# Kernel optimization log

Hardware: AMD Instinct MI355X
Metric: run time of the kernel (lower is better)

## Reference

```python
import jax, jax.numpy as jnp
import numpy as np

B, S, D, H = 4, 2048, 1024, 16
HD = D // H
EPS = 1e-5


def setup_inputs() -> dict:
    key = jax.random.key(0)
    ks = jax.random.split(key, 12)
    scale = 1.0 / np.sqrt(D)
    inp = {
        "x": jax.random.normal(ks[0], (B, S, D), dtype=jnp.float32),
        "template_ids": jax.random.randint(ks[1], (B, S), 0, 1000, dtype=jnp.int64)
            if jax.config.jax_enable_x64 else jax.random.randint(ks[1], (B, S), 0, 1000, dtype=jnp.int32),
        "attention_mask": jnp.ones((B, S), dtype=jnp.int32),
        "Wq": jax.random.normal(ks[2], (D, D), dtype=jnp.float32) * scale,
        "bq": jnp.zeros((D,), dtype=jnp.float32),
        "Wk": jax.random.normal(ks[3], (D, D), dtype=jnp.float32) * scale,
        "bk": jnp.zeros((D,), dtype=jnp.float32),
        "Wv": jax.random.normal(ks[4], (D, D), dtype=jnp.float32) * scale,
        "bv": jnp.zeros((D,), dtype=jnp.float32),
        "Wo": jax.random.normal(ks[5], (D, D), dtype=jnp.float32) * scale,
        "bo": jnp.zeros((D,), dtype=jnp.float32),
        "gamma": jnp.ones((D,), dtype=jnp.float32),
        "beta": jnp.zeros((D,), dtype=jnp.float32),
    }
    return inp


def _split_heads(t):
    # [B,S,D] -> [B,H,S,HD]
    return t.reshape(B, S, H, HD).transpose(0, 2, 1, 3)


def reference(x, template_ids, attention_mask, Wq, bq, Wk, bk, Wv, bv, Wo, bo, gamma, beta):
    q = _split_heads(x @ Wq.T + bq)
    k = _split_heads(x @ Wk.T + bk)
    v = _split_heads(x @ Wv.T + bv)
    # [B,H,S,S]
    scores = jnp.einsum("bhqd,bhkd->bhqk", q, k) / jnp.sqrt(jnp.float32(HD))
    mask = attention_mask[:, None, None, :]  # broadcast over heads and query dim
    scores = jnp.where(mask == 0, jnp.float32(-10000.0), scores)
    attn = jax.nn.softmax(scores, axis=-1)  # dropout is identity in eval
    out = jnp.einsum("bhqk,bhkd->bhqd", attn, v)
    out = out.transpose(0, 2, 1, 3).reshape(B, S, D)
    out = out @ Wo.T + bo
    # residual + LayerNorm
    y = x + out
    mu = jnp.mean(y, axis=-1, keepdims=True)
    var = jnp.var(y, axis=-1, keepdims=True)
    return (y - mu) * jax.lax.rsqrt(var + EPS) * gamma + beta
```

## Files before the change

kernel.cpp:

```cpp
#include <hip/hip_runtime.h>

typedef unsigned short u16;
typedef unsigned int u32;
typedef __attribute__((ext_vector_type(8))) short bf16x8;
typedef __attribute__((ext_vector_type(4))) float f32x4;

#define NB 4
#define SS 2048
#define DD 1024
#define NH 16
#define HD 64
#define MM (NB*SS)

struct __align__(16) Pack16 { unsigned int w0, w1, w2, w3; };
union PU { Pack16 p; u16 s[8]; };

__device__ __forceinline__ float b2f(u16 u) {
    union { unsigned int i; float f; } v; v.i = ((unsigned int)u) << 16; return v.f;
}
__device__ __forceinline__ u16 f2b(float f) {
    union { unsigned int i; float f; } v; v.f = f;
    return (u16)((v.i + 0x7FFFu + ((v.i >> 16) & 1u)) >> 16);
}
__device__ __forceinline__ u32 packbf(float a, float b) {
    u32 ia = __float_as_uint(a), ib = __float_as_uint(b);
    return ((ia + 0x8000u) >> 16) | ((ib + 0x8000u) & 0xFFFF0000u);
}
__device__ __forceinline__ float rdS(const void* p, size_t i, int mode) {
    return mode ? ((const float*)p)[i] : b2f(((const u16*)p)[i]);
}
__device__ __forceinline__ float ex2(float x) { return __builtin_amdgcn_exp2f(x); }

__device__ __forceinline__ void cp16(const u16* g, u16* l) {
    __builtin_amdgcn_global_load_lds(
        (const __attribute__((address_space(1))) void*)g,
        (__attribute__((address_space(3))) void*)l, 16, 0, 0);
}

__device__ __forceinline__ void pl32swap(u32& a, u32& b) {
    asm volatile("v_permlane32_swap_b32 %0, %1" : "+v"(a), "+v"(b));
}
__device__ __forceinline__ void pl16swap(u32& a, u32& b) {
    asm volatile("v_permlane16_swap_b32 %0, %1" : "+v"(a), "+v"(b));
}

#define QSC 0.1803368801111204f
#define GX ((size_t)MM * DD / 8)
#define GW ((size_t)DD * DD / 8)
#define GTOT (GX + 4 * GW + 512)

__global__ __launch_bounds__(256) void convert_kernel(
    const void* __restrict__ x,
    const void* __restrict__ Wq, const void* __restrict__ Wk,
    const void* __restrict__ Wv, const void* __restrict__ Wo,
    const void* __restrict__ bq, const void* __restrict__ bk,
    const void* __restrict__ bv, const void* __restrict__ bo,
    u16* __restrict__ xb, u16* __restrict__ Wc, u16* __restrict__ Wob,
    u16* __restrict__ bcat, const u32* __restrict__ gamma_w)
{
    const int mode = (gamma_w[0] == 0x3F800000u) ? 1 : 0;
    size_t g = (size_t)blockIdx.x * 256 + threadIdx.x;
    const void* src; u16* dst; size_t off; float sc = 1.0f;
    if (g < GX)               { src = x;  dst = xb;              off = g * 8; }
    else if (g < GX + GW)     { src = Wq; dst = Wc;              off = (g - GX) * 8; sc = QSC; }
    else if (g < GX + 2 * GW) { src = Wk; dst = Wc + (size_t)DD * DD;     off = (g - GX - GW) * 8; }
    else if (g < GX + 3 * GW) { src = Wv; dst = Wc + (size_t)2 * DD * DD; off = (g - GX - 2 * GW) * 8; }
    else if (g < GX + 4 * GW) { src = Wo; dst = Wob;             off = (g - GX - 3 * GW) * 8; }
    else {
        size_t gg = g - (GX + 4 * GW);
        int which = (int)(gg >> 7); off = (gg & 127) * 8;
        src = (which == 0) ? bq : (which == 1) ? bk : (which == 2) ? bv : bo;
        dst = bcat + which * DD;
        if (which == 0) sc = QSC;
    }
    PU o;
    if (mode) {
        const float* s = (const float*)src + off;
        float4 a = ((const float4*)s)[0];
        float4 b = ((const float4*)s)[1];
        o.s[0] = f2b(a.x * sc); o.s[1] = f2b(a.y * sc);
        o.s[2] = f2b(a.z * sc); o.s[3] = f2b(a.w * sc);
        o.s[4] = f2b(b.x * sc); o.s[5] = f2b(b.y * sc);
        o.s[6] = f2b(b.z * sc); o.s[7] = f2b(b.w * sc);
    } else {
        PU in; in.p = *(const Pack16*)((const u16*)src + off);
#pragma unroll
        for (int j = 0; j < 8; j++) o.s[j] = f2b(b2f(in.s[j]) * sc);
    }
    *(Pack16*)(dst + off) = o.p;
}

__global__ __launch_bounds__(256) void gemm_qkv(
    const u16* __restrict__ xb, const u16* __restrict__ Wc, const u16* __restrict__ bcat,
    u16* __restrict__ Q, u16* __restrict__ K, u16* __restrict__ V)
{
    __shared__ __align__(16) u16 sh[2 * 128 * 64];
    u16* As = sh;
    u16* Bs = sh + 128 * 64;

    const int tid  = threadIdx.x;
    const int wv   = tid >> 6;
    const int lane = tid & 63;
    const int wy = wv >> 1, wx = wv & 1;
    const int l15 = lane & 15, quad = lane >> 4;
    const int m0 = blockIdx.x * 128, n0 = blockIdx.y * 128;
    const int srow = lane >> 3;
    const int sw   = ((lane & 7) ^ srow) * 8;
    const int key  = l15 & 7;

    f32x4 acc[4][4];
#pragma unroll
    for (int i = 0; i < 4; i++)
#pragma unroll
        for (int j = 0; j < 4; j++) acc[i][j] = (f32x4){0.f, 0.f, 0.f, 0.f};

    for (int k0 = 0; k0 < DD; k0 += 64) {
#pragma unroll
        for (int c = 0; c < 4; c++) {
            cp16(&xb[(size_t)(m0 + wv * 32 + c * 8 + srow) * DD + k0 + sw],
                 &As[wv * 2048 + c * 512]);
            cp16(&Wc[(size_t)(n0 + wv * 32 + c * 8 + srow) * DD + k0 + sw],
                 &Bs[wv * 2048 + c * 512]);
        }
        __syncthreads();
#pragma unroll
        for (int ks = 0; ks < 2; ks++) {
            bf16x8 a[4], bb[4];
#pragma unroll
            for (int mt = 0; mt < 4; mt++)
                a[mt] = *(const bf16x8*)&As[(wy * 64 + mt * 16 + l15) * 64 +
                                            (((ks << 2) + quad) ^ key) * 8];
#pragma unroll
            for (int nt = 0; nt < 4; nt++)
                bb[nt] = *(const bf16x8*)&Bs[(wx * 64 + nt * 16 + l15) * 64 +
                                             (((ks << 2) + quad) ^ key) * 8];
#pragma unroll
            for (int mt = 0; mt < 4; mt++)
#pragma unroll
                for (int nt = 0; nt < 4; nt++)
                    acc[mt][nt] = __builtin_amdgcn_mfma_f32_16x16x32_bf16(
                        a[mt], bb[nt], acc[mt][nt], 0, 0, 0);
        }
        __syncthreads();
    }

    const int z = n0 >> 10;
    if (z != 2) {
        u16* out = (z == 0) ? Q : K;
#pragma unroll
        for (int nt = 0; nt < 4; nt++) {
            int n_g = n0 + wx * 64 + nt * 16 + l15;
            float bv_ = b2f(bcat[n_g]);
            int nn = n_g & 1023;
            int h = nn >> 6, hd = nn & 63;
#pragma unroll
            for (int mt = 0; mt < 4; mt++) {
#pragma unroll
                for (int r = 0; r < 4; r++) {
                    int m_g = m0 + wy * 64 + mt * 16 + quad * 4 + r;
                    int b = m_g >> 11, s = m_g & (SS - 1);
                    out[(((size_t)(b * NH + h) * SS) + s) * HD + hd] =
                        f2b(acc[mt][nt][r] + bv_);
                }
            }
        }
    } else {
        const int bb_ = m0 >> 11, sbase = m0 & (SS - 1);
#pragma unroll
        for (int ph = 0; ph < 2; ph++) {
            if (wx == ph) {
#pragma unroll
                for (int nt = 0; nt < 4; nt++) {
                    int n_loc = nt * 16 + l15;
                    float bv_ = b2f(bcat[n0 + ph * 64 + n_loc]);
#pragma unroll
                    for (int mt = 0; mt < 4; mt++) {
                        int m = wy * 64 + mt * 16 + quad * 4;
                        uint2 wr;
                        wr.x = (u32)f2b(acc[mt][nt][0] + bv_) |
                               ((u32)f2b(acc[mt][nt][1] + bv_) << 16);
                        wr.y = (u32)f2b(acc[mt][nt][2] + bv_) |
                               ((u32)f2b(acc[mt][nt][3] + bv_) << 16);
                        *(uint2*)&sh[n_loc * 136 + m] = wr;
                    }
                }
            }
            __syncthreads();
            {
                int row = tid >> 2;
                int sg  = tid & 3;
                int n_g = n0 + ph * 64 + row;
                int nn = n_g & 1023;
                int h = nn >> 6, hd = nn & 63;
                u16* dst = &V[(((size_t)(bb_ * NH + h)) * HD + hd) * SS + sbase];
#pragma unroll
                for (int j = 0; j < 4; j++) {
                    int mloc = sg * 32 + j * 8;
                    *(Pack16*)&dst[mloc] = *(const Pack16*)&sh[row * 136 + mloc];
                }
            }
            __syncthreads();
        }
    }
}

__global__ __launch_bounds__(256, 4) void attn_kernel(
    const u16* __restrict__ Q, const u16* __restrict__ K, const u16* __restrict__ V,
    const int* __restrict__ mask, u16* __restrict__ O)
{
    const int bh = blockIdx.y;
    const int b = bh >> 4, h = bh & 15;
    const int q0 = blockIdx.x * 128;
    const u16* Qp  = Q + (size_t)bh * SS * HD;
    const u16* Kp  = K + (size_t)bh * SS * HD;
    const u16* Vtg = V + (size_t)bh * HD * SS;
    const int* mk = mask + b * SS;

    __shared__ __align__(16) u16 Kl[2 * 64 * 64];
    __shared__ __align__(16) u16 Vt[2 * 64 * 64];
    __shared__ int s_anymask;

    const int tid  = threadIdx.x;
    const int w    = tid >> 6;
    const int lane = tid & 63;
    const int l15 = lane & 15, quad = lane >> 4;
    const int srow = lane >> 3;
    const int sw   = ((lane & 7) ^ srow) * 8;
    const int key  = l15 & 7;

    if (tid == 0) s_anymask = 0;
    __syncthreads();
    {
        int local = 0;
#pragma unroll
        for (int i = 0; i < 2; i++) {
            int4 m4 = ((const int4*)mk)[i * 256 + tid];
            if ((m4.x == 0) | (m4.y == 0) | (m4.z == 0) | (m4.w == 0)) local = 1;
        }
        if (local) s_anymask = 1;
    }
    __syncthreads();
    const bool anymask = (s_anymask != 0);

    bf16x8 qf[2][2];
#pragma unroll
    for (int qt = 0; qt < 2; qt++)
#pragma unroll
        for (int ks = 0; ks < 2; ks++)
            qf[qt][ks] = *(const bf16x8*)&Qp[(size_t)(q0 + w * 32 + qt * 16 + l15) * HD +
                                             ks * 32 + quad * 8];

    f32x4 oacc[2][4];
#pragma unroll
    for (int i = 0; i < 2; i++)
#pragma unroll
        for (int j = 0; j < 4; j++) oacc[i][j] = (f32x4){0.f, 0.f, 0.f, 0.f};

    float lsum[2] = {0.f, 0.f};

#pragma unroll
    for (int c = 0; c < 2; c++) {
        cp16(&Kp[(size_t)(w * 16 + c * 8 + srow) * HD + sw], &Kl[w * 1024 + c * 512]);
        cp16(&Vtg[(size_t)(w * 16 + c * 8 + srow) * SS + sw], &Vt[w * 1024 + c * 512]);
    }

    for (int it = 0; it < SS / 64; it++) {
        const int kv0 = it * 64;
        const int p = it & 1;
        __syncthreads();

        if (it + 1 < SS / 64) {
            const int kn = kv0 + 64;
#pragma unroll
            for (int c = 0; c < 2; c++) {
                cp16(&Kp[(size_t)(kn + w * 16 + c * 8 + srow) * HD + sw],
                     &Kl[(p ^ 1) * 4096 + w * 1024 + c * 512]);
                cp16(&Vtg[(size_t)(w * 16 + c * 8 + srow) * SS + kn + sw],
                     &Vt[(p ^ 1) * 4096 + w * 1024 + c * 512]);
            }
        }

        f32x4 sacc[4][2];
#pragma unroll
        for (int i = 0; i < 4; i++)
#pragma unroll
            for (int j = 0; j < 2; j++) sacc[i][j] = (f32x4){0.f, 0.f, 0.f, 0.f};
#pragma unroll
        for (int ks = 0; ks < 2; ks++) {
            bf16x8 kf[4];
#pragma unroll
            for (int kvt = 0; kvt < 4; kvt++)
                kf[kvt] = *(const bf16x8*)&Kl[p * 4096 + (kvt * 16 + l15) * 64 +
                                              (((ks << 2) + quad) ^ key) * 8];
            __builtin_amdgcn_s_setprio(1);
#pragma unroll
            for (int kvt = 0; kvt < 4; kvt++)
#pragma unroll
                for (int qt = 0; qt < 2; qt++)
                    sacc[kvt][qt] = __builtin_amdgcn_mfma_f32_16x16x32_bf16(
                        kf[kvt], qf[qt][ks], sacc[kvt][qt], 0, 0, 0);
            __builtin_amdgcn_s_setprio(0);
        }

        union { bf16x8 v; u32 d[4]; } paf[2][2];
#pragma unroll
        for (int qt = 0; qt < 2; qt++) {
            u32 pk[4][2];
#pragma unroll
            for (int kvt = 0; kvt < 4; kvt++) {
                f32x4 vv = sacc[kvt][qt];
                if (anymask) {
#pragma unroll
                    for (int r = 0; r < 4; r++) {
                        int kv = kv0 + kvt * 16 + quad * 4 + r;
                        if (mk[kv] == 0) vv[r] = -20000.0f;
                    }
                }
                float p0 = ex2(vv[0]);
                float p1 = ex2(vv[1]);
                float p2 = ex2(vv[2]);
                float p3 = ex2(vv[3]);
                lsum[qt] += (p0 + p1) + (p2 + p3);
                pk[kvt][0] = packbf(p0, p1);
                pk[kvt][1] = packbf(p2, p3);
            }
#pragma unroll
            for (int ks2 = 0; ks2 < 2; ks2++) {
#pragma unroll
                for (int c = 0; c < 2; c++) {
                    u32 x0 = pk[ks2 * 2 + 0][c];
                    u32 x1 = pk[ks2 * 2 + 1][c];
                    pl32swap(x0, x1);
                    pl16swap(x0, x1);
                    paf[qt][ks2].d[c]     = x0;
                    paf[qt][ks2].d[2 + c] = x1;
                }
            }
        }

#pragma unroll
        for (int ks2 = 0; ks2 < 2; ks2++) {
            bf16x8 vf[4];
#pragma unroll
            for (int nt = 0; nt < 4; nt++)
                vf[nt] = *(const bf16x8*)&Vt[p * 4096 + (nt * 16 + l15) * 64 +
                                             (((ks2 << 2) + quad) ^ key) * 8];
            __builtin_amdgcn_s_setprio(1);
#pragma unroll
            for (int qt = 0; qt < 2; qt++) {
#pragma unroll
                for (int nt = 0; nt < 4; nt++)
                    oacc[qt][nt] = __builtin_amdgcn_mfma_f32_16x16x32_bf16(
                        paf[qt][ks2].v, vf[nt], oacc[qt][nt], 0, 0, 0);
            }
            __builtin_amdgcn_s_setprio(0);
        }
    }

#pragma unroll
    for (int qt = 0; qt < 2; qt++) {
        lsum[qt] += __shfl_xor(lsum[qt], 16, 64);
        lsum[qt] += __shfl_xor(lsum[qt], 32, 64);
    }
#pragma unroll
    for (int qt = 0; qt < 2; qt++) {
#pragma unroll
        for (int r = 0; r < 4; r++) {
            float inv = 1.0f / __shfl(lsum[qt], quad * 4 + r, 64);
            int row = q0 + w * 32 + qt * 16 + quad * 4 + r;
            size_t base = ((size_t)(b * SS + row)) * DD + h * HD;
#pragma unroll
            for (int nt = 0; nt < 4; nt++)
                O[base + nt * 16 + l15] = f2b(oacc[qt][nt][r] * inv);
        }
    }
}

__global__ __launch_bounds__(256) void gemm_oproj(
    const u16* __restrict__ A, const u16* __restrict__ Wob, const u16* __restrict__ bcat,
    u16* __restrict__ Y)
{
    __shared__ __align__(16) u16 As[128 * 64];
    __shared__ __align__(16) u16 Bs[128 * 64];

    const int tid  = threadIdx.x;
    const int wv   = tid >> 6;
    const int lane = tid & 63;
    const int wy = wv >> 1, wx = wv & 1;
    const int l15 = lane & 15, quad = lane >> 4;
    const int m0 = blockIdx.x * 128, n0 = blockIdx.y * 128;
    const int srow = lane >> 3;
    const int sw   = ((lane & 7) ^ srow) * 8;
    const int key  = l15 & 7;

    f32x4 acc[4][4];
#pragma unroll
    for (int i = 0; i < 4; i++)
#pragma unroll
        for (int j = 0; j < 4; j++) acc[i][j] = (f32x4){0.f, 0.f, 0.f, 0.f};

    for (int k0 = 0; k0 < DD; k0 += 64) {
#pragma unroll
        for (int c = 0; c < 4; c++) {
            cp16(&A[(size_t)(m0 + wv * 32 + c * 8 + srow) * DD + k0 + sw],
                 &As[wv * 2048 + c * 512]);
            cp16(&Wob[(size_t)(n0 + wv * 32 + c * 8 + srow) * DD + k0 + sw],
                 &Bs[wv * 2048 + c * 512]);
        }
        __syncthreads();
#pragma unroll
        for (int ks = 0; ks < 2; ks++) {
            bf16x8 a[4], bb[4];
#pragma unroll
            for (int mt = 0; mt < 4; mt++)
                a[mt] = *(const bf16x8*)&As[(wy * 64 + mt * 16 + l15) * 64 +
                                            (((ks << 2) + quad) ^ key) * 8];
#pragma unroll
            for (int nt = 0; nt < 4; nt++)
                bb[nt] = *(const bf16x8*)&Bs[(wx * 64 + nt * 16 + l15) * 64 +
                                             (((ks << 2) + quad) ^ key) * 8];
#pragma unroll
            for (int mt = 0; mt < 4; mt++)
#pragma unroll
                for (int nt = 0; nt < 4; nt++)
                    acc[mt][nt] = __builtin_amdgcn_mfma_f32_16x16x32_bf16(
                        a[mt], bb[nt], acc[mt][nt], 0, 0, 0);
        }
        __syncthreads();
    }

#pragma unroll
    for (int nt = 0; nt < 4; nt++) {
        int n_g = n0 + wx * 64 + nt * 16 + l15;
        float bv_ = b2f(bcat[3 * DD + n_g]);
#pragma unroll
        for (int mt = 0; mt < 4; mt++) {
#pragma unroll
            for (int r = 0; r < 4; r++) {
                int m_g = m0 + wy * 64 + mt * 16 + quad * 4 + r;
                Y[(size_t)m_g * DD + n_g] = f2b(acc[mt][nt][r] + bv_);
            }
        }
    }
}

__global__ __launch_bounds__(256) void ln_kernel(
    const u16* __restrict__ Yp, const void* __restrict__ x,
    const void* __restrict__ gamma, const void* __restrict__ beta,
    void* __restrict__ out)
{
    const int mode = (((const u32*)gamma)[0] == 0x3F800000u) ? 1 : 0;
    const int w    = threadIdx.x >> 6;
    const int lane = threadIdx.x & 63;
    const int row  = blockIdx.x * 4 + w;
    const u16* y = Yp + (size_t)row * DD;

    float vals[16];
    float s = 0.f, sq = 0.f;
#pragma unroll
    for (int i = 0; i < 2; i++) {
        PU d; d.p = *(const Pack16*)&y[i * 512 + lane * 8];
        if (mode) {
            const float* xp = (const float*)x + (size_t)row * DD + i * 512 + lane * 8;
            float4 xa = ((const float4*)xp)[0];
            float4 xb2 = ((const float4*)xp)[1];
            float xr[8] = {xa.x, xa.y, xa.z, xa.w, xb2.x, xb2.y, xb2.z, xb2.w};
#pragma unroll
            for (int j = 0; j < 8; j++) {
                float f = b2f(d.s[j]) + xr[j];
                vals[i * 8 + j] = f;
                s += f; sq += f * f;
            }
        } else {
            const u16* xp = (const u16*)x + (size_t)row * DD + i * 512 + lane * 8;
            PU xd; xd.p = *(const Pack16*)xp;
#pragma unroll
            for (int j = 0; j < 8; j++) {
                float f = b2f(d.s[j]) + b2f(xd.s[j]);
                vals[i * 8 + j] = f;
                s += f; sq += f * f;
            }
        }
    }
#pragma unroll
    for (int off = 1; off < 64; off <<= 1) {
        s  += __shfl_xor(s, off);
        sq += __shfl_xor(sq, off);
    }
    float mu  = s * (1.0f / 1024.0f);
    float var = sq * (1.0f / 1024.0f) - mu * mu;
    float rs  = rsqrtf(var + 1e-5f);

#pragma unroll
    for (int i = 0; i < 2; i++) {
        float r8[8];
#pragma unroll
        for (int j = 0; j < 8; j++) {
            int col = i * 512 + lane * 8 + j;
            r8[j] = (vals[i * 8 + j] - mu) * rs * rdS(gamma, col, mode) + rdS(beta, col, mode);
        }
        if (mode) {
            float* of = (float*)out + (size_t)row * DD + i * 512 + lane * 8;
            ((float4*)of)[0] = make_float4(r8[0], r8[1], r8[2], r8[3]);
            ((float4*)of)[1] = make_float4(r8[4], r8[5], r8[6], r8[7]);
        } else {
            PU ob;
#pragma unroll
            for (int j = 0; j < 8; j++) ob.s[j] = f2b(r8[j]);
            *(Pack16*)((u16*)out + (size_t)row * DD + i * 512 + lane * 8) = ob.p;
        }
    }
}

extern "C" void kernel_launch(void* const* d_in, const int* in_sizes, int n_in,
                              void* d_out, int out_size, void* d_ws, size_t ws_size,
                              hipStream_t stream)
{
    const void* x     = d_in[0];
    const int* mask   = (const int*)d_in[2];
    const void* Wq    = d_in[3];
    const void* bq    = d_in[4];
    const void* Wk    = d_in[5];
    const void* bk    = d_in[6];
    const void* Wv    = d_in[7];
    const void* bv    = d_in[8];
    const void* Wo    = d_in[9];
    const void* bo    = d_in[10];
    const void* gamma = d_in[11];
    const void* beta  = d_in[12];

    const size_t n = (size_t)MM * DD;
    u16* xb   = (u16*)((char*)d_ws + 256);
    u16* Wc   = xb + n;
    u16* Wob  = Wc + (size_t)3 * DD * DD;
    u16* bcat = Wob + (size_t)DD * DD;
    u16* Qb   = bcat + 4096;
    u16* Kb   = Qb + n;
    u16* Vb   = Kb + n;
    u16* Ab   = Vb + n;
    u16* Yb   = xb;

    convert_kernel<<<(unsigned)(GTOT / 256), 256, 0, stream>>>(
        x, Wq, Wk, Wv, Wo, bq, bk, bv, bo, xb, Wc, Wob, bcat, (const u32*)gamma);
    gemm_qkv<<<dim3(MM / 128, 3 * DD / 128), 256, 0, stream>>>(xb, Wc, bcat, Qb, Kb, Vb);
    attn_kernel<<<dim3(SS / 128, NB * NH), 256, 0, stream>>>(Qb, Kb, Vb, mask, Ab);
    gemm_oproj<<<dim3(MM / 128, DD / 128), 256, 0, stream>>>(Ab, Wob, bcat, Yb);
    ln_kernel<<<MM / 4, 256, 0, stream>>>(Yb, x, gamma, beta, d_out);
}
```

Baseline: 327.5 us.

## Rewrite QKV and output GEMMs as 256x128 triple-buffered pipelined tiles

Replaces the two 128x128 single-buffered GEMM loops with a shared 256x128 tile routine run by 512 threads. It uses three LDS stages with async global-to-LDS loads two tiles ahead, split A/B staging, explicit vmcnt waits, sched barriers and setprio around the MFMA blocks. The grids are remapped with an XCD-aware block swizzle, and the V transpose epilogue is done in one pass. The aim is to hide global-load latency and raise reuse per block, at the cost of more LDS per block (144KB), lower occupancy and fragile hand-placed wait counts.

Result: slower. 351.2 us (+7.2%).

```diff
diff --git a/kernel.cpp b/kernel.cpp
--- a/kernel.cpp
+++ b/kernel.cpp
@@ -43,6 +43,8 @@
 __device__ __forceinline__ void pl16swap(u32& a, u32& b) {
     asm volatile("v_permlane16_swap_b32 %0, %1" : "+v"(a), "+v"(b));
 }
+
+#define SBAR __builtin_amdgcn_sched_barrier(0)
 
 #define QSC 0.1803368801111204f
 #define GX ((size_t)MM * DD / 8)
@@ -90,66 +92,133 @@
     *(Pack16*)(dst + off) = o.p;
 }
 
-__global__ __launch_bounds__(256) void gemm_qkv(
-    const u16* __restrict__ xb, const u16* __restrict__ Wc, const u16* __restrict__ bcat,
-    u16* __restrict__ Q, u16* __restrict__ K, u16* __restrict__ V)
-{
-    __shared__ __align__(16) u16 sh[2 * 128 * 64];
-    u16* As = sh;
-    u16* Bs = sh + 128 * 64;
-
+__device__ __forceinline__ void mfma_tile_256x128(
+    const u16* __restrict__ Ag,
+    const u16* __restrict__ Bg,
+    u16* sh, f32x4 (&acc)[4][4])
+{
     const int tid  = threadIdx.x;
     const int wv   = tid >> 6;
     const int lane = tid & 63;
-    const int wy = wv >> 1, wx = wv & 1;
+    const int wm = wv >> 1, wn = wv & 1;
     const int l15 = lane & 15, quad = lane >> 4;
-    const int m0 = blockIdx.x * 128, n0 = blockIdx.y * 128;
     const int srow = lane >> 3;
     const int sw   = ((lane & 7) ^ srow) * 8;
     const int key  = l15 & 7;
-
-    f32x4 acc[4][4];
-#pragma unroll
-    for (int i = 0; i < 4; i++)
-#pragma unroll
-        for (int j = 0; j < 4; j++) acc[i][j] = (f32x4){0.f, 0.f, 0.f, 0.f};
-
-    for (int k0 = 0; k0 < DD; k0 += 64) {
-#pragma unroll
-        for (int c = 0; c < 4; c++) {
-            cp16(&xb[(size_t)(m0 + wv * 32 + c * 8 + srow) * DD + k0 + sw],
-                 &As[wv * 2048 + c * 512]);
-            cp16(&Wc[(size_t)(n0 + wv * 32 + c * 8 + srow) * DD + k0 + sw],
-                 &Bs[wv * 2048 + c * 512]);
-        }
-        __syncthreads();
-#pragma unroll
-        for (int ks = 0; ks < 2; ks++) {
-            bf16x8 a[4], bb[4];
-#pragma unroll
-            for (int mt = 0; mt < 4; mt++)
-                a[mt] = *(const bf16x8*)&As[(wy * 64 + mt * 16 + l15) * 64 +
-                                            (((ks << 2) + quad) ^ key) * 8];
-#pragma unroll
-            for (int nt = 0; nt < 4; nt++)
-                bb[nt] = *(const bf16x8*)&Bs[(wx * 64 + nt * 16 + l15) * 64 +
-                                             (((ks << 2) + quad) ^ key) * 8];
-#pragma unroll
-            for (int mt = 0; mt < 4; mt++)
+    const int NT   = DD / 64;
+
+#define QSTAGE_A(tt, cc) do { \
+    const u16* s_ = Ag + (size_t)(tt) * 64; \
+    const int lb_ = (cc) * 24576 + wv * 1024; \
+    cp16(s_ + (size_t)(wv * 16 +           srow) * DD + sw, &sh[lb_]); \
+    cp16(s_ + (size_t)(wv * 16 + 8 +       srow) * DD + sw, &sh[lb_ + 512]); \
+    cp16(s_ + (size_t)(128 + wv * 16 +     srow) * DD + sw, &sh[lb_ + 8192]); \
+    cp16(s_ + (size_t)(128 + wv * 16 + 8 + srow) * DD + sw, &sh[lb_ + 8704]); \
+} while (0)
+#define QSTAGE_B(tt, cc) do { \
+    const u16* s_ = Bg + (size_t)(tt) * 64; \
+    const int lb_ = (cc) * 24576 + 16384 + wv * 1024; \
+    cp16(s_ + (size_t)(wv * 16 +     srow) * DD + sw, &sh[lb_]); \
+    cp16(s_ + (size_t)(wv * 16 + 8 + srow) * DD + sw, &sh[lb_ + 512]); \
+} while (0)
+
+    QSTAGE_A(0, 0); QSTAGE_B(0, 0);
+    QSTAGE_A(1, 1); QSTAGE_B(1, 1);
+    SBAR;
+    asm volatile("s_waitcnt vmcnt(6)");
+    __builtin_amdgcn_s_barrier();
+    SBAR;
+
+    int cb = 0;
+    for (int t = 0; t < NT; ++t) {
+        const int c2 = (cb >= 1) ? cb - 1 : 2;
+        const int ab = cb * 24576;
+        const int bb = ab + 16384;
+
+        bf16x8 bfr[4][2], afr[2][2];
+#pragma unroll
+        for (int nt = 0; nt < 4; nt++)
+#pragma unroll
+            for (int ks = 0; ks < 2; ks++)
+                bfr[nt][ks] = *(const bf16x8*)&sh[bb + (wn * 64 + nt * 16 + l15) * 64 +
+                                                  (((ks << 2) + quad) ^ key) * 8];
+#pragma unroll
+        for (int mt = 0; mt < 2; mt++)
+#pragma unroll
+            for (int ks = 0; ks < 2; ks++)
+                afr[mt][ks] = *(const bf16x8*)&sh[ab + (wm * 64 + mt * 16 + l15) * 64 +
+                                                  (((ks << 2) + quad) ^ key) * 8];
+        if (t + 2 < NT) QSTAGE_A(t + 2, c2);
+        SBAR; __builtin_amdgcn_s_barrier(); SBAR;
+        __builtin_amdgcn_s_setprio(1);
+#pragma unroll
+        for (int ks = 0; ks < 2; ks++)
+#pragma unroll
+            for (int mt = 0; mt < 2; mt++)
 #pragma unroll
                 for (int nt = 0; nt < 4; nt++)
                     acc[mt][nt] = __builtin_amdgcn_mfma_f32_16x16x32_bf16(
-                        a[mt], bb[nt], acc[mt][nt], 0, 0, 0);
-        }
-        __syncthreads();
-    }
+                        afr[mt][ks], bfr[nt][ks], acc[mt][nt], 0, 0, 0);
+        __builtin_amdgcn_s_setprio(0);
+        SBAR; __builtin_amdgcn_s_barrier(); SBAR;
+
+#pragma unroll
+        for (int mt = 0; mt < 2; mt++)
+#pragma unroll
+            for (int ks = 0; ks < 2; ks++)
+                afr[mt][ks] = *(const bf16x8*)&sh[ab + (wm * 64 + 32 + mt * 16 + l15) * 64 +
+                                                  (((ks << 2) + quad) ^ key) * 8];
+        if (t + 2 < NT) QSTAGE_B(t + 2, c2);
+        SBAR; __builtin_amdgcn_s_barrier(); SBAR;
+        __builtin_amdgcn_s_setprio(1);
+#pragma unroll
+        for (int ks = 0; ks < 2; ks++)
+#pragma unroll
+            for (int mt = 0; mt < 2; mt++)
+#pragma unroll
+                for (int nt = 0; nt < 4; nt++)
+                    acc[2 + mt][nt] = __builtin_amdgcn_mfma_f32_16x16x32_bf16(
+                        afr[mt][ks], bfr[nt][ks], acc[2 + mt][nt], 0, 0, 0);
+        __builtin_amdgcn_s_setprio(0);
+        SBAR;
+        if (t + 2 < NT)      asm volatile("s_waitcnt vmcnt(6)");
+        else if (t + 1 < NT) asm volatile("s_waitcnt vmcnt(0)");
+        __builtin_amdgcn_s_barrier();
+        SBAR;
+        cb = (cb == 2) ? 0 : cb + 1;
+    }
+#undef QSTAGE_A
+#undef QSTAGE_B
+}
+
+__global__ __launch_bounds__(512, 2) void gemm_qkv(
+    const u16* __restrict__ xb, const u16* __restrict__ Wc, const u16* __restrict__ bcat,
+    u16* __restrict__ Q, u16* __restrict__ K, u16* __restrict__ V)
+{
+    __shared__ __align__(16) u16 sh[3 * 24576];
+    const int wg = (blockIdx.x & 7) * 96 + (blockIdx.x >> 3);
+    const int mb = wg & 31, nb = wg >> 5;
+    const int m0 = mb * 256, n0 = nb * 128;
+
+    f32x4 acc[4][4];
+#pragma unroll
+    for (int i = 0; i < 4; i++)
+#pragma unroll
+        for (int j = 0; j < 4; j++) acc[i][j] = (f32x4){0.f, 0.f, 0.f, 0.f};
+
+    mfma_tile_256x128(xb + (size_t)m0 * DD, Wc + (size_t)n0 * DD, sh, acc);
+
+    const int tid = threadIdx.x;
+    const int wv = tid >> 6, lane = tid & 63;
+    const int wm = wv >> 1, wn = wv & 1;
+    const int l15 = lane & 15, quad = lane >> 4;
 
     const int z = n0 >> 10;
     if (z != 2) {
         u16* out = (z == 0) ? Q : K;
 #pragma unroll
         for (int nt = 0; nt < 4; nt++) {
-            int n_g = n0 + wx * 64 + nt * 16 + l15;
+            int n_g = n0 + wn * 64 + nt * 16 + l15;
             float bv_ = b2f(bcat[n_g]);
             int nn = n_g & 1023;
             int h = nn >> 6, hd = nn & 63;
@@ -157,7 +226,7 @@
             for (int mt = 0; mt < 4; mt++) {
 #pragma unroll
                 for (int r = 0; r < 4; r++) {
-                    int m_g = m0 + wy * 64 + mt * 16 + quad * 4 + r;
+                    int m_g = m0 + wm * 64 + mt * 16 + quad * 4 + r;
                     int b = m_g >> 11, s = m_g & (SS - 1);
                     out[(((size_t)(b * NH + h) * SS) + s) * HD + hd] =
                         f2b(acc[mt][nt][r] + bv_);
@@ -165,41 +234,36 @@
             }
         }
     } else {
-        const int bb_ = m0 >> 11, sbase = m0 & (SS - 1);
-#pragma unroll
-        for (int ph = 0; ph < 2; ph++) {
-            if (wx == ph) {
-#pragma unroll
-                for (int nt = 0; nt < 4; nt++) {
-                    int n_loc = nt * 16 + l15;
-                    float bv_ = b2f(bcat[n0 + ph * 64 + n_loc]);
-#pragma unroll
-                    for (int mt = 0; mt < 4; mt++) {
-                        int m = wy * 64 + mt * 16 + quad * 4;
-                        uint2 wr;
-                        wr.x = (u32)f2b(acc[mt][nt][0] + bv_) |
-                               ((u32)f2b(acc[mt][nt][1] + bv_) << 16);
-                        wr.y = (u32)f2b(acc[mt][nt][2] + bv_) |
-                               ((u32)f2b(acc[mt][nt][3] + bv_) << 16);
-                        *(uint2*)&sh[n_loc * 136 + m] = wr;
-                    }
-                }
-            }
-            __syncthreads();
-            {
-                int row = tid >> 2;
-                int sg  = tid & 3;
-                int n_g = n0 + ph * 64 + row;
-                int nn = n_g & 1023;
-                int h = nn >> 6, hd = nn & 63;
-                u16* dst = &V[(((size_t)(bb_ * NH + h)) * HD + hd) * SS + sbase];
-#pragma unroll
-                for (int j = 0; j < 4; j++) {
-                    int mloc = sg * 32 + j * 8;
-                    *(Pack16*)&dst[mloc] = *(const Pack16*)&sh[row * 136 + mloc];
-                }
-            }
-            __syncthreads();
+        __syncthreads();
+        const int bbk = m0 >> 11, sbase = m0 & (SS - 1);
+#pragma unroll
+        for (int nt = 0; nt < 4; nt++) {
+            int n_loc = wn * 64 + nt * 16 + l15;
+            float bv_ = b2f(bcat[n0 + n_loc]);
+#pragma unroll
+            for (int mt = 0; mt < 4; mt++) {
+                int m = wm * 64 + mt * 16 + quad * 4;
+                uint2 wr;
+                wr.x = (u32)f2b(acc[mt][nt][0] + bv_) |
+                       ((u32)f2b(acc[mt][nt][1] + bv_) << 16);
+                wr.y = (u32)f2b(acc[mt][nt][2] + bv_) |
+                       ((u32)f2b(acc[mt][nt][3] + bv_) << 16);
+                *(uint2*)&sh[n_loc * 264 + m] = wr;
+            }
+        }
+        __syncthreads();
+        {
+            int row = tid >> 2;
+            int sg  = tid & 3;
+            int n_g = n0 + row;
+            int nn = n_g & 1023;
+            int h = nn >> 6, hd = nn & 63;
+            u16* dst = &V[(((size_t)(bbk * NH + h)) * HD + hd) * SS + sbase];
+#pragma unroll
+            for (int j = 0; j < 8; j++) {
+                int mloc = sg * 64 + j * 8;
+                *(Pack16*)&dst[mloc] = *(const Pack16*)&sh[row * 264 + mloc];
+            }
         }
     }
 }
@@ -376,68 +440,37 @@
     }
 }
 
-__global__ __launch_bounds__(256) void gemm_oproj(
+__global__ __launch_bounds__(512, 2) void gemm_oproj(
     const u16* __restrict__ A, const u16* __restrict__ Wob, const u16* __restrict__ bcat,
     u16* __restrict__ Y)
 {
-    __shared__ __align__(16) u16 As[128 * 64];
-    __shared__ __align__(16) u16 Bs[128 * 64];
-
-    const int tid  = threadIdx.x;
-    const int wv   = tid >> 6;
-    const int lane = tid & 63;
-    const int wy = wv >> 1, wx = wv & 1;
+    __shared__ __align__(16) u16 sh[3 * 24576];
+    const int wg = (blockIdx.x & 7) * 32 + (blockIdx.x >> 3);
+    const int mb = wg & 31, nb = wg >> 5;
+    const int m0 = mb * 256, n0 = nb * 128;
+
+    f32x4 acc[4][4];
+#pragma unroll
+    for (int i = 0; i < 4; i++)
+#pragma unroll
+        for (int j = 0; j < 4; j++) acc[i][j] = (f32x4){0.f, 0.f, 0.f, 0.f};
+
+    mfma_tile_256x128(A + (size_t)m0 * DD, Wob + (size_t)n0 * DD, sh, acc);
+
+    const int tid = threadIdx.x;
+    const int wv = tid >> 6, lane = tid & 63;
+    const int wm = wv >> 1, wn = wv & 1;
     const int l15 = lane & 15, quad = lane >> 4;
-    const int m0 = blockIdx.x * 128, n0 = blockIdx.y * 128;
-    const int srow = lane >> 3;
-    const int sw   = ((lane & 7) ^ srow) * 8;
-    const int key  = l15 & 7;
-
-    f32x4 acc[4][4];
-#pragma unroll
-    for (int i = 0; i < 4; i++)
-#pragma unroll
-        for (int j = 0; j < 4; j++) acc[i][j] = (f32x4){0.f, 0.f, 0.f, 0.f};
-
-    for (int k0 = 0; k0 < DD; k0 += 64) {
-#pragma unroll
-        for (int c = 0; c < 4; c++) {
-            cp16(&A[(size_t)(m0 + wv * 32 + c * 8 + srow) * DD + k0 + sw],
-                 &As[wv * 2048 + c * 512]);
-            cp16(&Wob[(size_t)(n0 + wv * 32 + c * 8 + srow) * DD + k0 + sw],
-                 &Bs[wv * 2048 + c * 512]);
-        }
-        __syncthreads();
-#pragma unroll
-        for (int ks = 0; ks < 2; ks++) {
-            bf16x8 a[4], bb[4];
-#pragma unroll
-            for (int mt = 0; mt < 4; mt++)
-                a[mt] = *(const bf16x8*)&As[(wy * 64 + mt * 16 + l15) * 64 +
-                                            (((ks << 2) + quad) ^ key) * 8];
-#pragma unroll
-            for (int nt = 0; nt < 4; nt++)
-                bb[nt] = *(const bf16x8*)&Bs[(wx * 64 + nt * 16 + l15) * 64 +
-                                             (((ks << 2) + quad) ^ key) * 8];
-#pragma unroll
-            for (int mt = 0; mt < 4; mt++)
-#pragma unroll
-                for (int nt = 0; nt < 4; nt++)
-                    acc[mt][nt] = __builtin_amdgcn_mfma_f32_16x16x32_bf16(
-                        a[mt], bb[nt], acc[mt][nt], 0, 0, 0);
-        }
-        __syncthreads();
-    }
 
 #pragma unroll
     for (int nt = 0; nt < 4; nt++) {
-        int n_g = n0 + wx * 64 + nt * 16 + l15;
+        int n_g = n0 + wn * 64 + nt * 16 + l15;
         float bv_ = b2f(bcat[3 * DD + n_g]);
 #pragma unroll
         for (int mt = 0; mt < 4; mt++) {
 #pragma unroll
             for (int r = 0; r < 4; r++) {
-                int m_g = m0 + wy * 64 + mt * 16 + quad * 4 + r;
+                int m_g = m0 + wm * 64 + mt * 16 + quad * 4 + r;
                 Y[(size_t)m_g * DD + n_g] = f2b(acc[mt][nt][r] + bv_);
             }
         }
@@ -542,8 +575,8 @@
 
     convert_kernel<<<(unsigned)(GTOT / 256), 256, 0, stream>>>(
         x, Wq, Wk, Wv, Wo, bq, bk, bv, bo, xb, Wc, Wob, bcat, (const u32*)gamma);
-    gemm_qkv<<<dim3(MM / 128, 3 * DD / 128), 256, 0, stream>>>(xb, Wc, bcat, Qb, Kb, Vb);
+    gemm_qkv<<<768, 512, 0, stream>>>(xb, Wc, bcat, Qb, Kb, Vb);
     attn_kernel<<<dim3(SS / 128, NB * NH), 256, 0, stream>>>(Qb, Kb, Vb, mask, Ab);
-    gemm_oproj<<<dim3(MM / 128, DD / 128), 256, 0, stream>>>(Ab, Wob, bcat, Yb);
+    gemm_oproj<<<256, 512, 0, stream>>>(Ab, Wob, bcat, Yb);
     ln_kernel<<<MM / 4, 256, 0, stream>>>(Yb, x, gamma, beta, d_out);
 }
```
